# Kernel tuning notes

Hardware: AMD Instinct MI355X
Metric: run time of the kernel (lower is better)

The kernel has to match this reference:

```python
import jax, jax.numpy as jnp
import numpy as np

EPS = 1e-5  # BatchNorm eps
N_NODES, N_EDGES, F = 100000, 600000, 128


def setup_inputs() -> dict:
    key = jax.random.key(0)
    ks = jax.random.split(key, 16)
    inp = {
        "node_representations": jax.random.normal(ks[0], (N_NODES, F), jnp.float32),
        "edges": jax.random.randint(ks[1], (2, N_EDGES), 0, N_NODES, jnp.int64 if jax.config.jax_enable_x64 else jnp.int32),
        "edge_weights": jax.random.uniform(ks[2], (N_EDGES,), jnp.float32),
        # preprocess FFN: BatchNorm1d(F) [eval mode] + Linear(F, F) + GELU
        "pre_bn_gamma": jax.random.normal(ks[3], (F,), jnp.float32) * 0.1 + 1.0,
        "pre_bn_beta": jax.random.normal(ks[4], (F,), jnp.float32) * 0.1,
        "pre_bn_mean": jax.random.normal(ks[5], (F,), jnp.float32) * 0.1,
        "pre_bn_var": jax.random.uniform(ks[6], (F,), jnp.float32) * 0.5 + 0.5,
        "pre_w": jax.random.normal(ks[7], (F, F), jnp.float32) / np.sqrt(F),
        "pre_b": jnp.zeros((F,), jnp.float32),
        # update FFN: BatchNorm1d(2F) [eval mode] + Linear(2F, F) + GELU
        "upd_bn_gamma": jax.random.normal(ks[8], (2 * F,), jnp.float32) * 0.1 + 1.0,
        "upd_bn_beta": jax.random.normal(ks[9], (2 * F,), jnp.float32) * 0.1,
        "upd_bn_mean": jax.random.normal(ks[10], (2 * F,), jnp.float32) * 0.1,
        "upd_bn_var": jax.random.uniform(ks[11], (2 * F,), jnp.float32) * 0.5 + 0.5,
        "upd_w": jax.random.normal(ks[12], (2 * F, F), jnp.float32) / np.sqrt(2 * F),
        "upd_b": jnp.zeros((F,), jnp.float32),
    }
    return inp


def _bn_eval(x, gamma, beta, mean, var):
    return (x - mean) * (gamma / jnp.sqrt(var + EPS)) + beta


def reference(node_representations, edges, edge_weights,
              pre_bn_gamma, pre_bn_beta, pre_bn_mean, pre_bn_var, pre_w, pre_b,
              upd_bn_gamma, upd_bn_beta, upd_bn_mean, upd_bn_var, upd_w, upd_b):
    n_nodes, f = node_representations.shape
    node_idx, nbr_idx = edges[0], edges[1]
    # gather neighbour features: [E, F]
    x = node_representations[nbr_idx]
    # preprocess FFN (BN eval, dropout=identity in eval, linear, gelu)
    x = _bn_eval(x, pre_bn_gamma, pre_bn_beta, pre_bn_mean, pre_bn_var)
    x = jax.nn.gelu(x @ pre_w + pre_b, approximate=False)
    x = x * edge_weights[:, None]
    # mean aggregation (replicates torch.unique-on-expanded-indices counter = degree * F)
    agg = jax.ops.segment_sum(x, node_idx, num_segments=n_nodes)
    deg = jax.ops.segment_sum(jnp.ones_like(edge_weights), node_idx, num_segments=n_nodes)
    counter = (deg * f)[:, None]
    agg = jnp.where(counter > 0, agg / jnp.where(counter > 0, counter, 1.0), 0.0)
    # concat combine + update FFN
    emb = jnp.concatenate([node_representations, agg], axis=-1)
    emb = _bn_eval(emb, upd_bn_gamma, upd_bn_beta, upd_bn_mean, upd_bn_var)
    emb = jax.nn.gelu(emb @ upd_w + upd_b, approximate=False)
    return emb
```

## Files before the change

kernel.cpp:

```cpp
#include <hip/hip_runtime.h>
#include <math.h>

#define F 128
#define TWO_F 256
#define BN_EPS 1e-5f
#define PAD_A 136
#define PAD_A2 264

typedef unsigned short ushort_t;
typedef unsigned char uchar_t;
typedef __attribute__((ext_vector_type(8))) short bfrag;
typedef __attribute__((ext_vector_type(4))) float ffrag;
typedef __attribute__((ext_vector_type(2))) float floatx2;

__device__ __forceinline__ float gelu_exact(float x) {
    return 0.5f * x * (1.0f + erff(x * 0.70710678118654752f));
}
__device__ __forceinline__ ushort_t f2bf(float x) {
    unsigned int u = __float_as_uint(x);
    u = (u + 0x7FFFu + ((u >> 16) & 1u)) >> 16;
    return (ushort_t)u;
}
__device__ __forceinline__ unsigned int pk2(float a, float b) {
    return (unsigned int)f2bf(a) | ((unsigned int)f2bf(b) << 16);
}

__device__ __forceinline__ void fma4_fp8(float* acc, unsigned int d, float w) {
    floatx2 lo = __builtin_amdgcn_cvt_pk_f32_fp8(d, false);
    floatx2 hi = __builtin_amdgcn_cvt_pk_f32_fp8(d, true);
    acc[0] = fmaf(w, lo.x, acc[0]);
    acc[1] = fmaf(w, lo.y, acc[1]);
    acc[2] = fmaf(w, hi.x, acc[2]);
    acc[3] = fmaf(w, hi.y, acc[3]);
}
__device__ __forceinline__ void fma16_fp8(float* acc, uint4 a, float w) {
    fma4_fp8(acc + 0,  a.x, w); fma4_fp8(acc + 4,  a.y, w);
    fma4_fp8(acc + 8,  a.z, w); fma4_fp8(acc + 12, a.w, w);
}

__global__ __launch_bounds__(256) void prep(
    const float* __restrict__ pre_w, const float* __restrict__ pre_b,
    const float* __restrict__ g1, const float* __restrict__ be1,
    const float* __restrict__ m1, const float* __restrict__ v1,
    const float* __restrict__ upd_w, const float* __restrict__ upd_b,
    const float* __restrict__ g2, const float* __restrict__ be2,
    const float* __restrict__ m2, const float* __restrict__ v2,
    ushort_t* __restrict__ W1T, ushort_t* __restrict__ W2T,
    float* __restrict__ b1f, float* __restrict__ b2f,
    const int* __restrict__ edges, int* __restrict__ counts, int nEdges, int histBlocks) {
    const int t = threadIdx.x;
    if (blockIdx.x == 0) {
        __shared__ float t1[F], t2[TWO_F];
        if (t < F) {
            float s = g1[t] * rsqrtf(v1[t] + BN_EPS);
            t1[t] = be1[t] - m1[t] * s;
        }
        {
            float s = g2[t] * rsqrtf(v2[t] + BN_EPS);
            t2[t] = be2[t] - m2[t] * s;
        }
        __syncthreads();
        if (t < F) {
            float acc = pre_b[t];
            #pragma unroll 4
            for (int k = 0; k < F; ++k) acc = fmaf(t1[k], pre_w[k * F + t], acc);
            b1f[t] = acc;
        } else {
            int j = t - F;
            float acc = upd_b[j];
            #pragma unroll 4
            for (int k = 0; k < TWO_F; ++k) acc = fmaf(t2[k], upd_w[k * F + j], acc);
            b2f[j] = acc;
        }
    } else if (blockIdx.x <= 128) {
        int idx = (blockIdx.x - 1) * 256 + t;
        if (idx < F * F) {
            int k = idx & (F - 1), n = idx >> 7;
            float s = g1[k] * rsqrtf(v1[k] + BN_EPS);
            W1T[idx] = f2bf(s * pre_w[k * F + n]);
        }
        {
            int k = idx & (TWO_F - 1), n = idx >> 8;
            float s = g2[k] * rsqrtf(v2[k] + BN_EPS);
            W2T[idx] = f2bf(s * upd_w[k * F + n]);
        }
    } else {
        int b = blockIdx.x - 129;
        for (int i = b * 256 + t; i < nEdges; i += histBlocks * 256)
            atomicAdd(&counts[edges[i]], 1);
    }
}

__global__ __launch_bounds__(1024) void scan_pass1(const int* __restrict__ counts,
                                                   int* __restrict__ offsets,
                                                   int* __restrict__ blocksums, int n) {
    __shared__ int sb[1024];
    const int t = threadIdx.x;
    int idx = blockIdx.x * 1024 + t;
    int v = (idx < n) ? counts[idx] : 0;
    sb[t] = v;
    __syncthreads();
    for (int off = 1; off < 1024; off <<= 1) {
        int x = (t >= off) ? sb[t - off] : 0;
        __syncthreads();
        sb[t] += x;
        __syncthreads();
    }
    if (idx < n) offsets[idx + 1] = sb[t];
    if (t == 1023) blocksums[blockIdx.x] = sb[t];
}

__global__ __launch_bounds__(1024) void scan_pass3(const int* __restrict__ counts,
                                                   int* __restrict__ offsets,
                                                   const int* __restrict__ blocksums,
                                                   int* __restrict__ cursor, int n) {
    __shared__ int sb[1024];
    const int t = threadIdx.x;
    sb[t] = (t < blockIdx.x) ? blocksums[t] : 0;
    __syncthreads();
    #pragma unroll
    for (int off = 512; off > 0; off >>= 1) {
        if (t < off) sb[t] += sb[t + off];
        __syncthreads();
    }
    int base = sb[0];
    int idx = blockIdx.x * 1024 + t;
    if (idx < n) {
        int incl = offsets[idx + 1] + base;
        offsets[idx + 1] = incl;
        cursor[idx] = incl - counts[idx];
    }
    if (blockIdx.x == 0 && t == 0) offsets[0] = 0;
}

__global__ __launch_bounds__(256) void gemm1_fill(
    const float* __restrict__ nodes, const ushort_t* __restrict__ W1T,
    const float* __restrict__ b1f, uchar_t* __restrict__ G8, int nNodes,
    const int* __restrict__ edges, const float* __restrict__ ew,
    int* __restrict__ cursor, int2* __restrict__ csr, int nEdges,
    int gB, int fillBlocks) {
    __shared__ ushort_t As[64 * PAD_A];
    __shared__ float bs[F];
    const int t = threadIdx.x;

    if (blockIdx.x >= gB) {
        int b = blockIdx.x - gB;
        for (int e = b * 256 + t; e < nEdges; e += fillBlocks * 256) {
            int dst = edges[e];
            int pos = atomicAdd(&cursor[dst], 1);
            csr[pos] = make_int2(edges[nEdges + e], __float_as_int(ew[e]));
        }
        return;
    }

    const int base = blockIdx.x * 64;
    {
        int r = t >> 2, q = t & 3;
        int n = base + r;
        int sn = (n < nNodes) ? n : 0;
        const float4* src = reinterpret_cast<const float4*>(nodes + (size_t)sn * F + q * 32);
        uint4 pv[4];
        #pragma unroll
        for (int i = 0; i < 4; ++i) {
            float4 a = src[2 * i], b = src[2 * i + 1];
            pv[i].x = pk2(a.x, a.y); pv[i].y = pk2(a.z, a.w);
            pv[i].z = pk2(b.x, b.y); pv[i].w = pk2(b.z, b.w);
        }
        uint4* dst = reinterpret_cast<uint4*>(As + r * PAD_A + q * 32);
        #pragma unroll
        for (int i = 0; i < 4; ++i) dst[i] = pv[i];
    }
    if (t < F) bs[t] = b1f[t];
    __syncthreads();

    const int lane = t & 63, w = t >> 6;
    const int m = lane & 15, quad = lane >> 4;

    ffrag acc[8];
    #pragma unroll
    for (int c = 0; c < 8; ++c) acc[c] = (ffrag){0.f, 0.f, 0.f, 0.f};

    #pragma unroll
    for (int kk = 0; kk < 4; ++kk) {
        int k0 = kk * 32 + quad * 8;
        bfrag a = *reinterpret_cast<const bfrag*>(As + (w * 16 + m) * PAD_A + k0);
        #pragma unroll
        for (int c = 0; c < 8; ++c) {
            bfrag b = *reinterpret_cast<const bfrag*>(W1T + (size_t)(c * 16 + m) * F + k0);
            acc[c] = __builtin_amdgcn_mfma_f32_16x16x32_bf16(a, b, acc[c], 0, 0, 0);
        }
    }

    #pragma unroll
    for (int c = 0; c < 8; ++c) {
        int feat = c * 16 + m;
        float bj = bs[feat];
        #pragma unroll
        for (int i = 0; i < 4; ++i) {
            int n = base + w * 16 + quad * 4 + i;
            if (n < nNodes) {
                float v = gelu_exact(acc[c][i] + bj);
                int pkd = __builtin_amdgcn_cvt_pk_fp8_f32(v, v, 0, false);
                G8[(size_t)n * F + feat] = (uchar_t)(pkd & 0xFF);
            }
        }
    }
}

__global__ __launch_bounds__(256) void gather_agg(
    const uchar_t* __restrict__ G8, const int* __restrict__ offsets,
    const int2* __restrict__ csr, ushort_t* __restrict__ agg, int nNodes) {
    const int t = threadIdx.x;
    const int gid = blockIdx.x * 32 + (t >> 3);
    const int q = t & 7;
    if (gid >= nNodes) return;
    const int s = offsets[gid], e = offsets[gid + 1];

    float acc[16];
    #pragma unroll
    for (int j = 0; j < 16; ++j) acc[j] = 0.f;

    int i = s;
    while (i < e) {
        int c = e - i;
        c = (c > 8) ? 8 : c;
        uint4 av[8];
        float wv[8];
        #pragma unroll
        for (int j = 0; j < 8; ++j) {
            if (j < c) {
                int2 m = csr[i + j];
                wv[j] = __int_as_float(m.y);
                av[j] = *reinterpret_cast<const uint4*>(
                    G8 + (size_t)(unsigned int)m.x * F + q * 16);
            }
        }
        #pragma unroll
        for (int j = 0; j < 8; ++j)
            if (j < c) fma16_fp8(acc, av[j], wv[j]);
        i += c;
    }

    const int deg = e - s;
    const float inv = (deg > 0) ? 1.0f / ((float)deg * (float)F) : 0.f;
    uint4 pv0, pv1;
    pv0.x = pk2(acc[0] * inv, acc[1] * inv);  pv0.y = pk2(acc[2] * inv, acc[3] * inv);
    pv0.z = pk2(acc[4] * inv, acc[5] * inv);  pv0.w = pk2(acc[6] * inv, acc[7] * inv);
    pv1.x = pk2(acc[8] * inv, acc[9] * inv);  pv1.y = pk2(acc[10] * inv, acc[11] * inv);
    pv1.z = pk2(acc[12] * inv, acc[13] * inv); pv1.w = pk2(acc[14] * inv, acc[15] * inv);
    uint4* d = reinterpret_cast<uint4*>(agg + (size_t)gid * F + q * 16);
    d[0] = pv0; d[1] = pv1;
}

__global__ __launch_bounds__(256) void gemm2(
    const float* __restrict__ nodes, const ushort_t* __restrict__ agg,
    const ushort_t* __restrict__ W2T, const float* __restrict__ b2f,
    float* __restrict__ out, int nNodes) {
    __shared__ ushort_t As[64 * PAD_A2];
    __shared__ float bs[F];
    const int t = threadIdx.x;
    const int base = blockIdx.x * 64;

    {
        int r = t >> 2, q = t & 3;
        int n = base + r;
        int sn = (n < nNodes) ? n : 0;
        const float4* src = reinterpret_cast<const float4*>(nodes + (size_t)sn * F + q * 32);
        uint4 pv[4];
        #pragma unroll
        for (int i = 0; i < 4; ++i) {
            float4 a = src[2 * i], b = src[2 * i + 1];
            pv[i].x = pk2(a.x, a.y); pv[i].y = pk2(a.z, a.w);
            pv[i].z = pk2(b.x, b.y); pv[i].w = pk2(b.z, b.w);
        }
        uint4* dst = reinterpret_cast<uint4*>(As + r * PAD_A2 + q * 32);
        #pragma unroll
        for (int i = 0; i < 4; ++i) dst[i] = pv[i];
        const uint4* src2 = reinterpret_cast<const uint4*>(agg + (size_t)sn * F) + q * 4;
        uint4* dst2 = reinterpret_cast<uint4*>(As + r * PAD_A2 + F + q * 32);
        #pragma unroll
        for (int i = 0; i < 4; ++i) dst2[i] = src2[i];
    }
    if (t < F) bs[t] = b2f[t];
    __syncthreads();

    const int lane = t & 63, w = t >> 6;
    const int m = lane & 15, quad = lane >> 4;
    const int rg = w & 1, cg = w >> 1;

    ffrag acc0[4], acc1[4];
    #pragma unroll
    for (int c = 0; c < 4; ++c) {
        acc0[c] = (ffrag){0.f, 0.f, 0.f, 0.f};
        acc1[c] = (ffrag){0.f, 0.f, 0.f, 0.f};
    }

    #pragma unroll
    for (int kk = 0; kk < 8; ++kk) {
        int k0 = kk * 32 + quad * 8;
        bfrag a0 = *reinterpret_cast<const bfrag*>(As + (rg * 32 + m) * PAD_A2 + k0);
        bfrag a1 = *reinterpret_cast<const bfrag*>(As + (rg * 32 + 16 + m) * PAD_A2 + k0);
        #pragma unroll
        for (int c = 0; c < 4; ++c) {
            int feat = cg * 64 + c * 16 + m;
            bfrag b = *reinterpret_cast<const bfrag*>(W2T + (size_t)feat * TWO_F + k0);
            acc0[c] = __builtin_amdgcn_mfma_f32_16x16x32_bf16(a0, b, acc0[c], 0, 0, 0);
            acc1[c] = __builtin_amdgcn_mfma_f32_16x16x32_bf16(a1, b, acc1[c], 0, 0, 0);
        }
    }

    #pragma unroll
    for (int c = 0; c < 4; ++c) {
        int feat = cg * 64 + c * 16 + m;
        float bj = bs[feat];
        #pragma unroll
        for (int i = 0; i < 4; ++i) {
            int n0 = base + rg * 32 + quad * 4 + i;
            if (n0 < nNodes) out[(size_t)n0 * F + feat] = gelu_exact(acc0[c][i] + bj);
            int n1 = n0 + 16;
            if (n1 < nNodes) out[(size_t)n1 * F + feat] = gelu_exact(acc1[c][i] + bj);
        }
    }
}

extern "C" void kernel_launch(void* const* d_in, const int* in_sizes, int n_in,
                              void* d_out, int out_size, void* d_ws, size_t ws_size,
                              hipStream_t stream) {
    const float* nodes  = (const float*)d_in[0];
    const int*   edges  = (const int*)d_in[1];
    const float* ew     = (const float*)d_in[2];
    const float* pre_g  = (const float*)d_in[3];
    const float* pre_be = (const float*)d_in[4];
    const float* pre_m  = (const float*)d_in[5];
    const float* pre_v  = (const float*)d_in[6];
    const float* pre_w  = (const float*)d_in[7];
    const float* pre_b  = (const float*)d_in[8];
    const float* upd_g  = (const float*)d_in[9];
    const float* upd_be = (const float*)d_in[10];
    const float* upd_m  = (const float*)d_in[11];
    const float* upd_v  = (const float*)d_in[12];
    const float* upd_w  = (const float*)d_in[13];
    const float* upd_b  = (const float*)d_in[14];
    float* out = (float*)d_out;

    const int nNodes = in_sizes[0] / F;
    const int nEdges = in_sizes[2];
    const int nChunks = (nNodes + 1023) / 1024;
    const int histBlocks = 1024;
    const int gB = (nNodes + 63) / 64;
    const int fillBlocks = 1024;

    char* p = (char*)d_ws;
    int*      counts    = (int*)p;       p += (size_t)nNodes * 4;
    int*      offsets   = (int*)p;       p += (size_t)(nNodes + 4) * 4;
    int*      cursor    = (int*)p;       p += (size_t)nNodes * 4;
    int*      blocksums = (int*)p;       p += 1024 * 4;
    int2*     csr       = (int2*)p;      p += (size_t)nEdges * 8;
    float*    b1f       = (float*)p;     p += F * 4;
    float*    b2f       = (float*)p;     p += F * 4;
    ushort_t* W1T       = (ushort_t*)p;  p += F * F * 2;
    ushort_t* W2T       = (ushort_t*)p;  p += TWO_F * F * 2;
    uchar_t*  G8        = (uchar_t*)p;   p += (size_t)nNodes * F;
    ushort_t* agg       = (ushort_t*)p;

    hipMemsetAsync(counts, 0, (size_t)nNodes * 4, stream);

    prep<<<129 + histBlocks, 256, 0, stream>>>(
        pre_w, pre_b, pre_g, pre_be, pre_m, pre_v,
        upd_w, upd_b, upd_g, upd_be, upd_m, upd_v,
        W1T, W2T, b1f, b2f, edges, counts, nEdges, histBlocks);

    scan_pass1<<<nChunks, 1024, 0, stream>>>(counts, offsets, blocksums, nNodes);
    scan_pass3<<<nChunks, 1024, 0, stream>>>(counts, offsets, blocksums, cursor, nNodes);

    gemm1_fill<<<gB + fillBlocks, 256, 0, stream>>>(
        nodes, W1T, b1f, G8, nNodes, edges, ew, cursor, csr, nEdges, gB, fillBlocks);

    gather_agg<<<(nNodes + 31) / 32, 256, 0, stream>>>(
        G8, offsets, csr, agg, nNodes);

    gemm2<<<(nNodes + 63) / 64, 256, 0, stream>>>(
        nodes, agg, W2T, b2f, out, nNodes);
}
```

Baseline: 297.7 us.

## Pre-convert nodes to bf16, stage weights in LDS, persistent GEMM1, atomic-free CSR fill

Measured after the change: 267.8 us. 1.11x faster.

```diff
diff --git a/kernel.cpp b/kernel.cpp
--- a/kernel.cpp
+++ b/kernel.cpp
@@ -4,8 +4,8 @@
 #define F 128
 #define TWO_F 256
 #define BN_EPS 1e-5f
-#define PAD_A 136
-#define PAD_A2 264
+#define PAD_W1 136
+#define PAD_W2 264
 
 typedef unsigned short ushort_t;
 typedef unsigned char uchar_t;
@@ -47,7 +47,9 @@
     const float* __restrict__ m2, const float* __restrict__ v2,
     ushort_t* __restrict__ W1T, ushort_t* __restrict__ W2T,
     float* __restrict__ b1f, float* __restrict__ b2f,
-    const int* __restrict__ edges, int* __restrict__ counts, int nEdges, int histBlocks) {
+    const float* __restrict__ nodes, ushort_t* __restrict__ NB, int convB, int nNodes,
+    const int* __restrict__ edges, int* __restrict__ counts, int* __restrict__ rankb,
+    int nEdges, int histBlocks) {
     const int t = threadIdx.x;
     if (blockIdx.x == 0) {
         __shared__ float t1[F], t2[TWO_F];
@@ -84,10 +86,26 @@
             float s = g2[k] * rsqrtf(v2[k] + BN_EPS);
             W2T[idx] = f2bf(s * upd_w[k * F + n]);
         }
+    } else if (blockIdx.x <= 128 + convB) {
+        int cb = blockIdx.x - 129;
+        long long idx = (long long)cb * 4096 + t * 16;
+        if (idx < (long long)nNodes * F) {
+            const float4* s = reinterpret_cast<const float4*>(nodes + idx);
+            float4 f0 = s[0], f1 = s[1], f2 = s[2], f3 = s[3];
+            uint4 o0, o1;
+            o0.x = pk2(f0.x, f0.y); o0.y = pk2(f0.z, f0.w);
+            o0.z = pk2(f1.x, f1.y); o0.w = pk2(f1.z, f1.w);
+            o1.x = pk2(f2.x, f2.y); o1.y = pk2(f2.z, f2.w);
+            o1.z = pk2(f3.x, f3.y); o1.w = pk2(f3.z, f3.w);
+            uint4* d = reinterpret_cast<uint4*>(NB + idx);
+            d[0] = o0; d[1] = o1;
+        }
     } else {
-        int b = blockIdx.x - 129;
-        for (int i = b * 256 + t; i < nEdges; i += histBlocks * 256)
-            atomicAdd(&counts[edges[i]], 1);
+        int b = blockIdx.x - 129 - convB;
+        for (int i = b * 256 + t; i < nEdges; i += histBlocks * 256) {
+            int rk = atomicAdd(&counts[edges[i]], 1);
+            rankb[i] = rk;
+        }
     }
 }
 
@@ -134,75 +152,80 @@
 }
 
 __global__ __launch_bounds__(256) void gemm1_fill(
-    const float* __restrict__ nodes, const ushort_t* __restrict__ W1T,
+    const ushort_t* __restrict__ NB, const ushort_t* __restrict__ W1T,
     const float* __restrict__ b1f, uchar_t* __restrict__ G8, int nNodes,
     const int* __restrict__ edges, const float* __restrict__ ew,
-    int* __restrict__ cursor, int2* __restrict__ csr, int nEdges,
-    int gB, int fillBlocks) {
-    __shared__ ushort_t As[64 * PAD_A];
-    __shared__ float bs[F];
-    const int t = threadIdx.x;
-
-    if (blockIdx.x >= gB) {
-        int b = blockIdx.x - gB;
+    const int* __restrict__ offsets, const int* __restrict__ rankb,
+    int2* __restrict__ csr, int nEdges,
+    int gemmBlocks, int fillBlocks, int nTiles) {
+    __shared__ ushort_t Wl[F * PAD_W1];
+    __shared__ float bsm[F];
+    __shared__ uchar_t bounce[4][16 * F];
+    const int t = threadIdx.x;
+
+    if (blockIdx.x >= gemmBlocks) {
+        int b = blockIdx.x - gemmBlocks;
         for (int e = b * 256 + t; e < nEdges; e += fillBlocks * 256) {
             int dst = edges[e];
-            int pos = atomicAdd(&cursor[dst], 1);
+            int pos = offsets[dst] + rankb[e];
             csr[pos] = make_int2(edges[nEdges + e], __float_as_int(ew[e]));
         }
         return;
     }
 
-    const int base = blockIdx.x * 64;
-    {
-        int r = t >> 2, q = t & 3;
-        int n = base + r;
-        int sn = (n < nNodes) ? n : 0;
-        const float4* src = reinterpret_cast<const float4*>(nodes + (size_t)sn * F + q * 32);
-        uint4 pv[4];
-        #pragma unroll
-        for (int i = 0; i < 4; ++i) {
-            float4 a = src[2 * i], b = src[2 * i + 1];
-            pv[i].x = pk2(a.x, a.y); pv[i].y = pk2(a.z, a.w);
-            pv[i].z = pk2(b.x, b.y); pv[i].w = pk2(b.z, b.w);
-        }
-        uint4* dst = reinterpret_cast<uint4*>(As + r * PAD_A + q * 32);
-        #pragma unroll
-        for (int i = 0; i < 4; ++i) dst[i] = pv[i];
-    }
-    if (t < F) bs[t] = b1f[t];
+    for (int j = t; j < 2048; j += 256) {
+        int feat = j >> 4, kc = j & 15;
+        *reinterpret_cast<uint4*>(Wl + feat * PAD_W1 + kc * 8) =
+            reinterpret_cast<const uint4*>(W1T)[j];
+    }
+    if (t < F) bsm[t] = b1f[t];
     __syncthreads();
 
     const int lane = t & 63, w = t >> 6;
     const int m = lane & 15, quad = lane >> 4;
-
-    ffrag acc[8];
-    #pragma unroll
-    for (int c = 0; c < 8; ++c) acc[c] = (ffrag){0.f, 0.f, 0.f, 0.f};
-
-    #pragma unroll
-    for (int kk = 0; kk < 4; ++kk) {
-        int k0 = kk * 32 + quad * 8;
-        bfrag a = *reinterpret_cast<const bfrag*>(As + (w * 16 + m) * PAD_A + k0);
+    const int rr = lane >> 2, cc = (lane & 3) * 32;
+
+    for (int tile = blockIdx.x; tile < nTiles; tile += gemmBlocks) {
+        const int tb = tile * 64;
+        int arow = tb + w * 16 + m;
+        if (arow >= nNodes) arow = 0;
+        const ushort_t* ap = NB + (size_t)arow * F + quad * 8;
+
+        bfrag a[4];
+        #pragma unroll
+        for (int kk = 0; kk < 4; ++kk)
+            a[kk] = *reinterpret_cast<const bfrag*>(ap + kk * 32);
+
+        ffrag acc[8];
+        #pragma unroll
+        for (int c = 0; c < 8; ++c) acc[c] = (ffrag){0.f, 0.f, 0.f, 0.f};
+
+        #pragma unroll
+        for (int kk = 0; kk < 4; ++kk) {
+            int k0 = kk * 32 + quad * 8;
+            #pragma unroll
+            for (int c = 0; c < 8; ++c) {
+                bfrag b = *reinterpret_cast<const bfrag*>(Wl + (c * 16 + m) * PAD_W1 + k0);
+                acc[c] = __builtin_amdgcn_mfma_f32_16x16x32_bf16(a[kk], b, acc[c], 0, 0, 0);
+            }
+        }
+
         #pragma unroll
         for (int c = 0; c < 8; ++c) {
-            bfrag b = *reinterpret_cast<const bfrag*>(W1T + (size_t)(c * 16 + m) * F + k0);
-            acc[c] = __builtin_amdgcn_mfma_f32_16x16x32_bf16(a, b, acc[c], 0, 0, 0);
-        }
-    }
-
-    #pragma unroll
-    for (int c = 0; c < 8; ++c) {
-        int feat = c * 16 + m;
-        float bj = bs[feat];
-        #pragma unroll
-        for (int i = 0; i < 4; ++i) {
-            int n = base + w * 16 + quad * 4 + i;
-            if (n < nNodes) {
+            float bj = bsm[c * 16 + m];
+            #pragma unroll
+            for (int i = 0; i < 4; ++i) {
                 float v = gelu_exact(acc[c][i] + bj);
                 int pkd = __builtin_amdgcn_cvt_pk_fp8_f32(v, v, 0, false);
-                G8[(size_t)n * F + feat] = (uchar_t)(pkd & 0xFF);
+                bounce[w][(quad * 4 + i) * F + c * 16 + m] = (uchar_t)(pkd & 0xFF);
             }
+        }
+        uint4 d0 = *reinterpret_cast<const uint4*>(&bounce[w][rr * F + cc]);
+        uint4 d1 = *reinterpret_cast<const uint4*>(&bounce[w][rr * F + cc + 16]);
+        int gr = tb + w * 16 + rr;
+        if (gr < nNodes) {
+            *reinterpret_cast<uint4*>(G8 + (size_t)gr * F + cc) = d0;
+            *reinterpret_cast<uint4*>(G8 + (size_t)gr * F + cc + 16) = d1;
         }
     }
 }
@@ -252,45 +275,38 @@
     d[0] = pv0; d[1] = pv1;
 }
 
-__global__ __launch_bounds__(256) void gemm2(
-    const float* __restrict__ nodes, const ushort_t* __restrict__ agg,
+__global__ __launch_bounds__(512, 4) void gemm2(
+    const ushort_t* __restrict__ NB, const ushort_t* __restrict__ agg,
     const ushort_t* __restrict__ W2T, const float* __restrict__ b2f,
     float* __restrict__ out, int nNodes) {
-    __shared__ ushort_t As[64 * PAD_A2];
-    __shared__ float bs[F];
-    const int t = threadIdx.x;
-    const int base = blockIdx.x * 64;
-
-    {
-        int r = t >> 2, q = t & 3;
-        int n = base + r;
-        int sn = (n < nNodes) ? n : 0;
-        const float4* src = reinterpret_cast<const float4*>(nodes + (size_t)sn * F + q * 32);
-        uint4 pv[4];
-        #pragma unroll
-        for (int i = 0; i < 4; ++i) {
-            float4 a = src[2 * i], b = src[2 * i + 1];
-            pv[i].x = pk2(a.x, a.y); pv[i].y = pk2(a.z, a.w);
-            pv[i].z = pk2(b.x, b.y); pv[i].w = pk2(b.z, b.w);
-        }
-        uint4* dst = reinterpret_cast<uint4*>(As + r * PAD_A2 + q * 32);
-        #pragma unroll
-        for (int i = 0; i < 4; ++i) dst[i] = pv[i];
-        const uint4* src2 = reinterpret_cast<const uint4*>(agg + (size_t)sn * F) + q * 4;
-        uint4* dst2 = reinterpret_cast<uint4*>(As + r * PAD_A2 + F + q * 32);
-        #pragma unroll
-        for (int i = 0; i < 4; ++i) dst2[i] = src2[i];
-    }
-    if (t < F) bs[t] = b2f[t];
+    __shared__ ushort_t Wl[F * PAD_W2];
+    __shared__ float bsm[F];
+    const int t = threadIdx.x;
+
+    for (int j = t; j < 4096; j += 512) {
+        int feat = j >> 5, kc = j & 31;
+        *reinterpret_cast<uint4*>(Wl + feat * PAD_W2 + kc * 8) =
+            reinterpret_cast<const uint4*>(W2T)[j];
+    }
+    if (t < F) bsm[t] = b2f[t];
     __syncthreads();
 
     const int lane = t & 63, w = t >> 6;
     const int m = lane & 15, quad = lane >> 4;
-    const int rg = w & 1, cg = w >> 1;
-
-    ffrag acc0[4], acc1[4];
+    const int tb = blockIdx.x * 256;
+
+    int row0 = tb + w * 32 + m;
+    int row1 = row0 + 16;
+    int r0c = (row0 < nNodes) ? row0 : 0;
+    int r1c = (row1 < nNodes) ? row1 : 0;
+    const ushort_t* p0n = NB  + (size_t)r0c * F + quad * 8;
+    const ushort_t* p1n = NB  + (size_t)r1c * F + quad * 8;
+    const ushort_t* p0a = agg + (size_t)r0c * F + quad * 8;
+    const ushort_t* p1a = agg + (size_t)r1c * F + quad * 8;
+
+    ffrag acc0[8], acc1[8];
     #pragma unroll
-    for (int c = 0; c < 4; ++c) {
+    for (int c = 0; c < 8; ++c) {
         acc0[c] = (ffrag){0.f, 0.f, 0.f, 0.f};
         acc1[c] = (ffrag){0.f, 0.f, 0.f, 0.f};
     }
@@ -298,24 +314,27 @@
     #pragma unroll
     for (int kk = 0; kk < 8; ++kk) {
         int k0 = kk * 32 + quad * 8;
-        bfrag a0 = *reinterpret_cast<const bfrag*>(As + (rg * 32 + m) * PAD_A2 + k0);
-        bfrag a1 = *reinterpret_cast<const bfrag*>(As + (rg * 32 + 16 + m) * PAD_A2 + k0);
-        #pragma unroll
-        for (int c = 0; c < 4; ++c) {
-            int feat = cg * 64 + c * 16 + m;
-            bfrag b = *reinterpret_cast<const bfrag*>(W2T + (size_t)feat * TWO_F + k0);
+        bfrag a0 = (kk < 4)
+            ? *reinterpret_cast<const bfrag*>(p0n + kk * 32)
+            : *reinterpret_cast<const bfrag*>(p0a + (kk - 4) * 32);
+        bfrag a1 = (kk < 4)
+            ? *reinterpret_cast<const bfrag*>(p1n + kk * 32)
+            : *reinterpret_cast<const bfrag*>(p1a + (kk - 4) * 32);
+        #pragma unroll
+        for (int c = 0; c < 8; ++c) {
+            bfrag b = *reinterpret_cast<const bfrag*>(Wl + (c * 16 + m) * PAD_W2 + k0);
             acc0[c] = __builtin_amdgcn_mfma_f32_16x16x32_bf16(a0, b, acc0[c], 0, 0, 0);
             acc1[c] = __builtin_amdgcn_mfma_f32_16x16x32_bf16(a1, b, acc1[c], 0, 0, 0);
         }
     }
 
     #pragma unroll
-    for (int c = 0; c < 4; ++c) {
-        int feat = cg * 64 + c * 16 + m;
-        float bj = bs[feat];
+    for (int c = 0; c < 8; ++c) {
+        int feat = c * 16 + m;
+        float bj = bsm[feat];
         #pragma unroll
         for (int i = 0; i < 4; ++i) {
-            int n0 = base + rg * 32 + quad * 4 + i;
+            int n0 = tb + w * 32 + quad * 4 + i;
             if (n0 < nNodes) out[(size_t)n0 * F + feat] = gelu_exact(acc0[c][i] + bj);
             int n1 = n0 + 16;
             if (n1 < nNodes) out[(size_t)n1 * F + feat] = gelu_exact(acc1[c][i] + bj);
@@ -347,8 +366,10 @@
     const int nEdges = in_sizes[2];
     const int nChunks = (nNodes + 1023) / 1024;
     const int histBlocks = 1024;
-    const int gB = (nNodes + 63) / 64;
-    const int fillBlocks = 1024;
+    const int convB = (int)(((long long)nNodes * F + 4095) / 4096);
+    const int gemmBlocks = 768;
+    const int fillBlocks = 512;
+    const int nTiles = (nNodes + 63) / 64;
 
     char* p = (char*)d_ws;
     int*      counts    = (int*)p;       p += (size_t)nNodes * 4;
@@ -361,24 +382,28 @@
     ushort_t* W1T       = (ushort_t*)p;  p += F * F * 2;
     ushort_t* W2T       = (ushort_t*)p;  p += TWO_F * F * 2;
     uchar_t*  G8        = (uchar_t*)p;   p += (size_t)nNodes * F;
-    ushort_t* agg       = (ushort_t*)p;
+    ushort_t* agg       = (ushort_t*)p;  p += (size_t)nNodes * F * 2;
+    int*      rankb     = (int*)p;       p += (size_t)nEdges * 4;
+    ushort_t* NB        = (ushort_t*)p;
 
     hipMemsetAsync(counts, 0, (size_t)nNodes * 4, stream);
 
-    prep<<<129 + histBlocks, 256, 0, stream>>>(
+    prep<<<129 + convB + histBlocks, 256, 0, stream>>>(
         pre_w, pre_b, pre_g, pre_be, pre_m, pre_v,
         upd_w, upd_b, upd_g, upd_be, upd_m, upd_v,
-        W1T, W2T, b1f, b2f, edges, counts, nEdges, histBlocks);
+        W1T, W2T, b1f, b2f, nodes, NB, convB, nNodes,
+        edges, counts, rankb, nEdges, histBlocks);
 
     scan_pass1<<<nChunks, 1024, 0, stream>>>(counts, offsets, blocksums, nNodes);
     scan_pass3<<<nChunks, 1024, 0, stream>>>(counts, offsets, blocksums, cursor, nNodes);
 
-    gemm1_fill<<<gB + fillBlocks, 256, 0, stream>>>(
-        nodes, W1T, b1f, G8, nNodes, edges, ew, cursor, csr, nEdges, gB, fillBlocks);
+    gemm1_fill<<<gemmBlocks + fillBlocks, 256, 0, stream>>>(
+        NB, W1T, b1f, G8, nNodes, edges, ew, offsets, rankb, csr, nEdges,
+        gemmBlocks, fillBlocks, nTiles);
 
     gather_agg<<<(nNodes + 31) / 32, 256, 0, stream>>>(
         G8, offsets, csr, agg, nNodes);
 
-    gemm2<<<(nNodes + 63) / 64, 256, 0, stream>>>(
-        nodes, agg, W2T, b2f, out, nNodes);
-}
+    gemm2<<<(nNodes + 255) / 256, 512, 0, stream>>>(
+        NB, agg, W2T, b2f, out, nNodes);
+}
```
